# Optimization experiments

Measured on AMD Instinct MI355X. Metric: run time of the kernel, lower is better.

Reference implementation:

```python
import jax, jax.numpy as jnp
import numpy as np

N_NODES = 100000
N_EDGES = 1600000
D_FEAT = 64


def setup_inputs() -> dict:
    key = jax.random.key(0)
    k1, k2, k3, k4 = jax.random.split(key, 4)
    x = jax.random.normal(k1, (N_NODES, D_FEAT), dtype=jnp.float32)
    edge_values = jax.random.uniform(k2, (N_EDGES,), dtype=jnp.float32)
    # row-sorted targets mimic a coalesced sparse COO matrix
    target_index = jnp.sort(jax.random.randint(k3, (N_EDGES,), 0, N_NODES, dtype=jnp.int32))
    source_index = jax.random.randint(k4, (N_EDGES,), 0, N_NODES, dtype=jnp.int32)
    return {"x": x, "edge_values": edge_values,
            "target_index": target_index, "source_index": source_index}


def reference(x, edge_values, target_index, source_index):
    # sparsify_message: gather source rows -> [n_edges, d]
    msg = x[source_index]
    # scale by sparse neighborhood values
    msg = edge_values[:, None] * msg
    # aggregate: scatter-sum into target cells -> [n_nodes, d]
    out = jax.ops.segment_sum(msg, target_index, num_segments=N_NODES)
    return out
```

## Files before the change

kernel.cpp:

```cpp
#include <hip/hip_runtime.h>
#include <hip/hip_fp16.h>

#define N_NODES 100000
#define N_EDGES 1600000
#define D_FEAT 64

typedef __attribute__((ext_vector_type(4))) _Float16 half4v;

__global__ __launch_bounds__(256) void prep_kernel(
    const float4* __restrict__ x4,
    const int*    __restrict__ tgt,
    half4v*       __restrict__ xh,
    int*          __restrict__ row_ptr,
    int conv_blocks)
{
    const int bid = blockIdx.x;
    if (bid < conv_blocks) {
        int i = bid * 256 + threadIdx.x;
        if (i < N_NODES * 16) {
            float4 v = x4[i];
            half4v h;
            h.x = (_Float16)v.x; h.y = (_Float16)v.y;
            h.z = (_Float16)v.z; h.w = (_Float16)v.w;
            xh[i] = h;
        }
    } else {
        int e = (bid - conv_blocks) * 256 + threadIdx.x;
        if (e >= N_EDGES) return;
        int cur = tgt[e];
        int lo  = (e == 0) ? 0 : tgt[e - 1] + 1;
        for (int n = lo; n <= cur; ++n) row_ptr[n] = e;
        if (e == N_EDGES - 1) {
            for (int n = cur + 1; n <= N_NODES; ++n) row_ptr[n] = N_EDGES;
        }
    }
}

__global__ __launch_bounds__(256) void build_row_ptr(
    const int* __restrict__ tgt, int* __restrict__ row_ptr)
{
    int e = blockIdx.x * blockDim.x + threadIdx.x;
    if (e >= N_EDGES) return;
    int cur = tgt[e];
    int lo  = (e == 0) ? 0 : tgt[e - 1] + 1;
    for (int n = lo; n <= cur; ++n) row_ptr[n] = e;
    if (e == N_EDGES - 1) {
        for (int n = cur + 1; n <= N_NODES; ++n) row_ptr[n] = N_EDGES;
    }
}

__global__ __launch_bounds__(256) void gather_sum_h(
    const half4v* __restrict__ xh,
    const float*  __restrict__ ev,
    const int*    __restrict__ src,
    const int*    __restrict__ row_ptr,
    float4*       __restrict__ out4)
{
    const int node = blockIdx.x * 4 + (threadIdx.x >> 6);
    if (node >= N_NODES) return;
    const int lane = threadIdx.x & 63;
    const int g    = lane >> 4;
    const int f    = lane & 15;

    const int start = row_ptr[node];
    const int end   = row_ptr[node + 1];

    float4 acc = make_float4(0.f, 0.f, 0.f, 0.f);

    if (start < end) {
        int  ea = start + g, eb = start + 4 + g;
        bool va = ea < end,  vb = eb < end;
        int  esa = va ? ea : start, esb = vb ? eb : start;
        float wa = va ? ev[esa] : 0.0f;
        float wb = vb ? ev[esb] : 0.0f;
        int   sa = src[esa];
        int   sb = src[esb];

        for (int e0 = start; e0 < end; e0 += 8) {
            const half4v xa = xh[sa * 16 + f];
            const half4v xb = xh[sb * 16 + f];
            const float cwa = wa, cwb = wb;

            {
                int  na = e0 + 8 + g, nb = e0 + 12 + g;
                bool vna = na < end,  vnb = nb < end;
                int  nsa = vna ? na : start, nsb = vnb ? nb : start;
                wa = vna ? ev[nsa] : 0.0f;
                wb = vnb ? ev[nsb] : 0.0f;
                sa = src[nsa];
                sb = src[nsb];
            }

            acc.x = fmaf(cwa, (float)xa.x, acc.x);
            acc.y = fmaf(cwa, (float)xa.y, acc.y);
            acc.z = fmaf(cwa, (float)xa.z, acc.z);
            acc.w = fmaf(cwa, (float)xa.w, acc.w);
            acc.x = fmaf(cwb, (float)xb.x, acc.x);
            acc.y = fmaf(cwb, (float)xb.y, acc.y);
            acc.z = fmaf(cwb, (float)xb.z, acc.z);
            acc.w = fmaf(cwb, (float)xb.w, acc.w);
        }
    }

    acc.x += __shfl_xor(acc.x, 16, 64);
    acc.y += __shfl_xor(acc.y, 16, 64);
    acc.z += __shfl_xor(acc.z, 16, 64);
    acc.w += __shfl_xor(acc.w, 16, 64);
    acc.x += __shfl_xor(acc.x, 32, 64);
    acc.y += __shfl_xor(acc.y, 32, 64);
    acc.z += __shfl_xor(acc.z, 32, 64);
    acc.w += __shfl_xor(acc.w, 32, 64);

    if (g == 0) out4[node * 16 + f] = acc;
}

__global__ __launch_bounds__(256) void gather_sum_f32(
    const float4* __restrict__ x4,
    const float*  __restrict__ ev,
    const int*    __restrict__ src,
    const int*    __restrict__ row_ptr,
    float4*       __restrict__ out4)
{
    const int node = blockIdx.x * 4 + (threadIdx.x >> 6);
    if (node >= N_NODES) return;
    const int lane = threadIdx.x & 63;
    const int g    = lane >> 4;
    const int f    = lane & 15;

    const int start = row_ptr[node];
    const int end   = row_ptr[node + 1];

    float4 acc = make_float4(0.f, 0.f, 0.f, 0.f);
    if (start < end) {
        int  ea = start + g, eb = start + 4 + g;
        bool va = ea < end,  vb = eb < end;
        int  esa = va ? ea : start, esb = vb ? eb : start;
        float wa = va ? ev[esa] : 0.0f;
        float wb = vb ? ev[esb] : 0.0f;
        int   sa = src[esa];
        int   sb = src[esb];

        for (int e0 = start; e0 < end; e0 += 8) {
            const float4 xa = x4[sa * 16 + f];
            const float4 xb = x4[sb * 16 + f];
            const float cwa = wa, cwb = wb;
            {
                int  na = e0 + 8 + g, nb = e0 + 12 + g;
                bool vna = na < end,  vnb = nb < end;
                int  nsa = vna ? na : start, nsb = vnb ? nb : start;
                wa = vna ? ev[nsa] : 0.0f;
                wb = vnb ? ev[nsb] : 0.0f;
                sa = src[nsa];
                sb = src[nsb];
            }
            acc.x = fmaf(cwa, xa.x, acc.x);
            acc.y = fmaf(cwa, xa.y, acc.y);
            acc.z = fmaf(cwa, xa.z, acc.z);
            acc.w = fmaf(cwa, xa.w, acc.w);
            acc.x = fmaf(cwb, xb.x, acc.x);
            acc.y = fmaf(cwb, xb.y, acc.y);
            acc.z = fmaf(cwb, xb.z, acc.z);
            acc.w = fmaf(cwb, xb.w, acc.w);
        }
    }
    acc.x += __shfl_xor(acc.x, 16, 64);
    acc.y += __shfl_xor(acc.y, 16, 64);
    acc.z += __shfl_xor(acc.z, 16, 64);
    acc.w += __shfl_xor(acc.w, 16, 64);
    acc.x += __shfl_xor(acc.x, 32, 64);
    acc.y += __shfl_xor(acc.y, 32, 64);
    acc.z += __shfl_xor(acc.z, 32, 64);
    acc.w += __shfl_xor(acc.w, 32, 64);
    if (g == 0) out4[node * 16 + f] = acc;
}

extern "C" void kernel_launch(void* const* d_in, const int* in_sizes, int n_in,
                              void* d_out, int out_size, void* d_ws, size_t ws_size,
                              hipStream_t stream) {
    const float* x            = (const float*)d_in[0];
    const float* edge_values  = (const float*)d_in[1];
    const int*   target_index = (const int*)d_in[2];
    const int*   source_index = (const int*)d_in[3];
    float*       out          = (float*)d_out;

    const size_t rp_bytes = (size_t)(N_NODES + 1) * sizeof(int);
    const size_t xh_off   = (rp_bytes + 511) & ~(size_t)511;
    const size_t xh_bytes = (size_t)N_NODES * D_FEAT * sizeof(_Float16);
    const size_t need     = xh_off + xh_bytes;

    int* row_ptr = (int*)d_ws;

    if (ws_size >= need) {
        half4v* xh = (half4v*)((char*)d_ws + xh_off);
        const int conv_blocks = (N_NODES * 16 + 255) / 256;
        const int rp_blocks   = (N_EDGES + 255) / 256;
        prep_kernel<<<conv_blocks + rp_blocks, 256, 0, stream>>>(
            (const float4*)x, target_index, xh, row_ptr, conv_blocks);

        gather_sum_h<<<(N_NODES + 3) / 4, 256, 0, stream>>>(
            xh, edge_values, source_index, row_ptr, (float4*)out);
    } else {
        build_row_ptr<<<(N_EDGES + 255) / 256, 256, 0, stream>>>(target_index, row_ptr);
        gather_sum_f32<<<(N_NODES + 3) / 4, 256, 0, stream>>>(
            (const float4*)x, edge_values, source_index, row_ptr, (float4*)out);
    }
}
```

Measured before the change: 134.5 us.

## Map one 16-lane group per node and stage edge metadata through LDS

The half-precision gather kernel now assigns a 16-thread group to each node (16 nodes per block) in place of a full 64-lane wavefront. Each group loads up to 16 edges' source indices and weights cooperatively, stages them in shared memory, then issues four row gathers per step with software prefetching. This removes the cross-group shuffle reduction and the idle lanes on low-degree nodes, and quadruples nodes per block. In exchange each lane walks the edges serially, and the LDS exchange relies on implicit intra-wavefront ordering with no barrier.

```diff
diff --git a/kernel.cpp b/kernel.cpp
--- a/kernel.cpp
+++ b/kernel.cpp
@@ -49,6 +49,9 @@
     }
 }
 
+#define GROUPS_PER_BLOCK 16
+#define LDS_STRIDE_B     144
+
 __global__ __launch_bounds__(256) void gather_sum_h(
     const half4v* __restrict__ xh,
     const float*  __restrict__ ev,
@@ -56,62 +59,88 @@
     const int*    __restrict__ row_ptr,
     float4*       __restrict__ out4)
 {
-    const int node = blockIdx.x * 4 + (threadIdx.x >> 6);
+    __shared__ char lds_raw[GROUPS_PER_BLOCK * LDS_STRIDE_B];
+
+    const int tib  = threadIdx.x;
+    const int gib  = tib >> 4;
+    const int lane = tib & 15;
+    const int node = blockIdx.x * GROUPS_PER_BLOCK + gib;
     if (node >= N_NODES) return;
-    const int lane = threadIdx.x & 63;
-    const int g    = lane >> 4;
-    const int f    = lane & 15;
+
+    char* gbase = lds_raw + gib * LDS_STRIDE_B;
 
     const int start = row_ptr[node];
     const int end   = row_ptr[node + 1];
 
     float4 acc = make_float4(0.f, 0.f, 0.f, 0.f);
 
-    if (start < end) {
-        int  ea = start + g, eb = start + 4 + g;
-        bool va = ea < end,  vb = eb < end;
-        int  esa = va ? ea : start, esb = vb ? eb : start;
-        float wa = va ? ev[esa] : 0.0f;
-        float wb = vb ? ev[esb] : 0.0f;
-        int   sa = src[esa];
-        int   sb = src[esb];
-
-        for (int e0 = start; e0 < end; e0 += 8) {
-            const half4v xa = xh[sa * 16 + f];
-            const half4v xb = xh[sb * 16 + f];
-            const float cwa = wa, cwb = wb;
-
-            {
-                int  na = e0 + 8 + g, nb = e0 + 12 + g;
-                bool vna = na < end,  vnb = nb < end;
-                int  nsa = vna ? na : start, nsb = vnb ? nb : start;
-                wa = vna ? ev[nsa] : 0.0f;
-                wb = vnb ? ev[nsb] : 0.0f;
-                sa = src[nsa];
-                sb = src[nsb];
-            }
-
-            acc.x = fmaf(cwa, (float)xa.x, acc.x);
-            acc.y = fmaf(cwa, (float)xa.y, acc.y);
-            acc.z = fmaf(cwa, (float)xa.z, acc.z);
-            acc.w = fmaf(cwa, (float)xa.w, acc.w);
-            acc.x = fmaf(cwb, (float)xb.x, acc.x);
-            acc.y = fmaf(cwb, (float)xb.y, acc.y);
-            acc.z = fmaf(cwb, (float)xb.z, acc.z);
-            acc.w = fmaf(cwb, (float)xb.w, acc.w);
-        }
-    }
-
-    acc.x += __shfl_xor(acc.x, 16, 64);
-    acc.y += __shfl_xor(acc.y, 16, 64);
-    acc.z += __shfl_xor(acc.z, 16, 64);
-    acc.w += __shfl_xor(acc.w, 16, 64);
-    acc.x += __shfl_xor(acc.x, 32, 64);
-    acc.y += __shfl_xor(acc.y, 32, 64);
-    acc.z += __shfl_xor(acc.z, 32, 64);
-    acc.w += __shfl_xor(acc.w, 32, 64);
-
-    if (g == 0) out4[node * 16 + f] = acc;
+    for (int blk = start; blk < end; blk += 16) {
+        const int bcnt = end - blk;
+
+        int   s_ = 0; float w_ = 0.0f;
+        if (lane < bcnt) { s_ = src[blk + lane]; w_ = ev[blk + lane]; }
+        ((int2*)gbase)[lane] = make_int2(s_, __float_as_int(w_));
+
+        const int nch = (min(bcnt, 16) + 3) >> 2;
+
+        int4 m01 = ((const int4*)gbase)[0];
+        int4 m23 = ((const int4*)gbase)[1];
+        half4v x0 = xh[m01.x * 16 + lane];
+        half4v x1 = xh[m01.z * 16 + lane];
+        half4v x2 = xh[m23.x * 16 + lane];
+        half4v x3 = xh[m23.z * 16 + lane];
+        float w0 = __int_as_float(m01.y), w1 = __int_as_float(m01.w);
+        float w2 = __int_as_float(m23.y), w3 = __int_as_float(m23.w);
+
+        for (int c = 1; c < nch; ++c) {
+            int4 n01 = ((const int4*)gbase)[2 * c];
+            int4 n23 = ((const int4*)gbase)[2 * c + 1];
+            half4v nx0 = xh[n01.x * 16 + lane];
+            half4v nx1 = xh[n01.z * 16 + lane];
+            half4v nx2 = xh[n23.x * 16 + lane];
+            half4v nx3 = xh[n23.z * 16 + lane];
+
+            acc.x = fmaf(w0, (float)x0.x, acc.x);
+            acc.y = fmaf(w0, (float)x0.y, acc.y);
+            acc.z = fmaf(w0, (float)x0.z, acc.z);
+            acc.w = fmaf(w0, (float)x0.w, acc.w);
+            acc.x = fmaf(w1, (float)x1.x, acc.x);
+            acc.y = fmaf(w1, (float)x1.y, acc.y);
+            acc.z = fmaf(w1, (float)x1.z, acc.z);
+            acc.w = fmaf(w1, (float)x1.w, acc.w);
+            acc.x = fmaf(w2, (float)x2.x, acc.x);
+            acc.y = fmaf(w2, (float)x2.y, acc.y);
+            acc.z = fmaf(w2, (float)x2.z, acc.z);
+            acc.w = fmaf(w2, (float)x2.w, acc.w);
+            acc.x = fmaf(w3, (float)x3.x, acc.x);
+            acc.y = fmaf(w3, (float)x3.y, acc.y);
+            acc.z = fmaf(w3, (float)x3.z, acc.z);
+            acc.w = fmaf(w3, (float)x3.w, acc.w);
+
+            x0 = nx0; x1 = nx1; x2 = nx2; x3 = nx3;
+            w0 = __int_as_float(n01.y); w1 = __int_as_float(n01.w);
+            w2 = __int_as_float(n23.y); w3 = __int_as_float(n23.w);
+        }
+
+        acc.x = fmaf(w0, (float)x0.x, acc.x);
+        acc.y = fmaf(w0, (float)x0.y, acc.y);
+        acc.z = fmaf(w0, (float)x0.z, acc.z);
+        acc.w = fmaf(w0, (float)x0.w, acc.w);
+        acc.x = fmaf(w1, (float)x1.x, acc.x);
+        acc.y = fmaf(w1, (float)x1.y, acc.y);
+        acc.z = fmaf(w1, (float)x1.z, acc.z);
+        acc.w = fmaf(w1, (float)x1.w, acc.w);
+        acc.x = fmaf(w2, (float)x2.x, acc.x);
+        acc.y = fmaf(w2, (float)x2.y, acc.y);
+        acc.z = fmaf(w2, (float)x2.z, acc.z);
+        acc.w = fmaf(w2, (float)x2.w, acc.w);
+        acc.x = fmaf(w3, (float)x3.x, acc.x);
+        acc.y = fmaf(w3, (float)x3.y, acc.y);
+        acc.z = fmaf(w3, (float)x3.z, acc.z);
+        acc.w = fmaf(w3, (float)x3.w, acc.w);
+    }
+
+    out4[node * 16 + lane] = acc;
 }
 
 __global__ __launch_bounds__(256) void gather_sum_f32(
@@ -197,7 +226,8 @@
         prep_kernel<<<conv_blocks + rp_blocks, 256, 0, stream>>>(
             (const float4*)x, target_index, xh, row_ptr, conv_blocks);
 
-        gather_sum_h<<<(N_NODES + 3) / 4, 256, 0, stream>>>(
+        const int n_blocks = (N_NODES + GROUPS_PER_BLOCK - 1) / GROUPS_PER_BLOCK;
+        gather_sum_h<<<n_blocks, 256, 0, stream>>>(
             xh, edge_values, source_index, row_ptr, (float4*)out);
     } else {
         build_row_ptr<<<(N_EDGES + 255) / 256, 256, 0, stream>>>(target_index, row_ptr);
```

Result: faster. 120.8 us, median of 2 (-10.2%).

## Use 8-lane groups per node with LDS-staged edge indices and half8 gathers

Applied to the files above, without the earlier changes.

Changes the fp16 gather kernel from 64 lanes per node to 8 lanes per node, so each block handles 32 nodes and each lane loads 16-byte half8 vectors. Source indices and weights for up to 32 edges are loaded cooperatively and staged in LDS, then walked with a software-pipelined loop that prefetches the next four rows. The cross-lane shuffle reduction goes away, and far fewer lanes sit idle on nodes with few edges (about 16 per node). In exchange there is LDS traffic, per-lane serial loops over edges, and no explicit barrier around the LDS use (each 8-lane group uses only its own slice).

```diff
diff --git a/kernel.cpp b/kernel.cpp
--- a/kernel.cpp
+++ b/kernel.cpp
@@ -6,6 +6,7 @@
 #define D_FEAT 64
 
 typedef __attribute__((ext_vector_type(4))) _Float16 half4v;
+typedef __attribute__((ext_vector_type(8))) _Float16 half8v;
 
 __global__ __launch_bounds__(256) void prep_kernel(
     const float4* __restrict__ x4,
@@ -49,69 +50,101 @@
     }
 }
 
-__global__ __launch_bounds__(256) void gather_sum_h(
-    const half4v* __restrict__ xh,
+#define GPB        32
+#define LDS_STRIDE 272
+
+__global__ __launch_bounds__(256, 8) void gather_sum_h(
+    const half8v* __restrict__ xh8,
     const float*  __restrict__ ev,
     const int*    __restrict__ src,
     const int*    __restrict__ row_ptr,
     float4*       __restrict__ out4)
 {
-    const int node = blockIdx.x * 4 + (threadIdx.x >> 6);
+    __shared__ char lds_raw[GPB * LDS_STRIDE];
+
+    const int tib  = threadIdx.x;
+    const int gib  = tib >> 3;
+    const int lane = tib & 7;
+    const int node = blockIdx.x * GPB + gib;
     if (node >= N_NODES) return;
-    const int lane = threadIdx.x & 63;
-    const int g    = lane >> 4;
-    const int f    = lane & 15;
+
+    char* gbase = lds_raw + gib * LDS_STRIDE;
 
     const int start = row_ptr[node];
     const int end   = row_ptr[node + 1];
 
-    float4 acc = make_float4(0.f, 0.f, 0.f, 0.f);
-
-    if (start < end) {
-        int  ea = start + g, eb = start + 4 + g;
-        bool va = ea < end,  vb = eb < end;
-        int  esa = va ? ea : start, esb = vb ? eb : start;
-        float wa = va ? ev[esa] : 0.0f;
-        float wb = vb ? ev[esb] : 0.0f;
-        int   sa = src[esa];
-        int   sb = src[esb];
-
-        for (int e0 = start; e0 < end; e0 += 8) {
-            const half4v xa = xh[sa * 16 + f];
-            const half4v xb = xh[sb * 16 + f];
-            const float cwa = wa, cwb = wb;
-
-            {
-                int  na = e0 + 8 + g, nb = e0 + 12 + g;
-                bool vna = na < end,  vnb = nb < end;
-                int  nsa = vna ? na : start, nsb = vnb ? nb : start;
-                wa = vna ? ev[nsa] : 0.0f;
-                wb = vnb ? ev[nsb] : 0.0f;
-                sa = src[nsa];
-                sb = src[nsb];
-            }
-
-            acc.x = fmaf(cwa, (float)xa.x, acc.x);
-            acc.y = fmaf(cwa, (float)xa.y, acc.y);
-            acc.z = fmaf(cwa, (float)xa.z, acc.z);
-            acc.w = fmaf(cwa, (float)xa.w, acc.w);
-            acc.x = fmaf(cwb, (float)xb.x, acc.x);
-            acc.y = fmaf(cwb, (float)xb.y, acc.y);
-            acc.z = fmaf(cwb, (float)xb.z, acc.z);
-            acc.w = fmaf(cwb, (float)xb.w, acc.w);
-        }
-    }
-
-    acc.x += __shfl_xor(acc.x, 16, 64);
-    acc.y += __shfl_xor(acc.y, 16, 64);
-    acc.z += __shfl_xor(acc.z, 16, 64);
-    acc.w += __shfl_xor(acc.w, 16, 64);
-    acc.x += __shfl_xor(acc.x, 32, 64);
-    acc.y += __shfl_xor(acc.y, 32, 64);
-    acc.z += __shfl_xor(acc.z, 32, 64);
-    acc.w += __shfl_xor(acc.w, 32, 64);
-
-    if (g == 0) out4[node * 16 + f] = acc;
+    float4 accA = make_float4(0.f, 0.f, 0.f, 0.f);
+    float4 accB = make_float4(0.f, 0.f, 0.f, 0.f);
+
+#define ACC8(W, X) do { \
+        accA.x = fmaf((W), (float)(X)[0], accA.x); \
+        accA.y = fmaf((W), (float)(X)[1], accA.y); \
+        accA.z = fmaf((W), (float)(X)[2], accA.z); \
+        accA.w = fmaf((W), (float)(X)[3], accA.w); \
+        accB.x = fmaf((W), (float)(X)[4], accB.x); \
+        accB.y = fmaf((W), (float)(X)[5], accB.y); \
+        accB.z = fmaf((W), (float)(X)[6], accB.z); \
+        accB.w = fmaf((W), (float)(X)[7], accB.w); } while (0)
+
+    for (int blk = start; blk < end; blk += 32) {
+        {
+            const int e0   = blk + 4 * lane;
+            const int emax = end - 1;
+            int c0 = e0     < emax ? e0     : emax;
+            int c1 = e0 + 1 < emax ? e0 + 1 : emax;
+            int c2 = e0 + 2 < emax ? e0 + 2 : emax;
+            int c3 = e0 + 3 < emax ? e0 + 3 : emax;
+            int s0 = src[c0], s1 = src[c1], s2 = src[c2], s3 = src[c3];
+            float w0 = ev[c0], w1 = ev[c1], w2 = ev[c2], w3 = ev[c3];
+            w0 = (e0     < end) ? w0 : 0.0f;
+            w1 = (e0 + 1 < end) ? w1 : 0.0f;
+            w2 = (e0 + 2 < end) ? w2 : 0.0f;
+            w3 = (e0 + 3 < end) ? w3 : 0.0f;
+            ((int4*)gbase)[2 * lane]     =
+                make_int4(s0, __float_as_int(w0), s1, __float_as_int(w1));
+            ((int4*)gbase)[2 * lane + 1] =
+                make_int4(s2, __float_as_int(w2), s3, __float_as_int(w3));
+        }
+
+        const int rem = end - blk;
+        const int nch = ((rem < 32 ? rem : 32) + 3) >> 2;
+
+        int4 p0 = ((const int4*)gbase)[0];
+        int4 p1 = ((const int4*)gbase)[1];
+        half8v xa0 = xh8[p0.x * 8 + lane];
+        half8v xb0 = xh8[p0.z * 8 + lane];
+        half8v xc0 = xh8[p1.x * 8 + lane];
+        half8v xd0 = xh8[p1.z * 8 + lane];
+
+        for (int c = 1; c < nch; ++c) {
+            int4 q0 = ((const int4*)gbase)[2 * c];
+            int4 q1 = ((const int4*)gbase)[2 * c + 1];
+            half8v xa1 = xh8[q0.x * 8 + lane];
+            half8v xb1 = xh8[q0.z * 8 + lane];
+            half8v xc1 = xh8[q1.x * 8 + lane];
+            half8v xd1 = xh8[q1.z * 8 + lane];
+
+            int4 m0 = ((const int4*)gbase)[2 * (c - 1)];
+            int4 m1 = ((const int4*)gbase)[2 * (c - 1) + 1];
+            ACC8(__int_as_float(m0.y), xa0);
+            ACC8(__int_as_float(m0.w), xb0);
+            ACC8(__int_as_float(m1.y), xc0);
+            ACC8(__int_as_float(m1.w), xd0);
+
+            xa0 = xa1; xb0 = xb1; xc0 = xc1; xd0 = xd1;
+        }
+
+        int4 m0 = ((const int4*)gbase)[2 * (nch - 1)];
+        int4 m1 = ((const int4*)gbase)[2 * (nch - 1) + 1];
+        ACC8(__int_as_float(m0.y), xa0);
+        ACC8(__int_as_float(m0.w), xb0);
+        ACC8(__int_as_float(m1.y), xc0);
+        ACC8(__int_as_float(m1.w), xd0);
+    }
+#undef ACC8
+
+    out4[node * 16 + lane * 2]     = accA;
+    out4[node * 16 + lane * 2 + 1] = accB;
 }
 
 __global__ __launch_bounds__(256) void gather_sum_f32(
@@ -197,8 +230,9 @@
         prep_kernel<<<conv_blocks + rp_blocks, 256, 0, stream>>>(
             (const float4*)x, target_index, xh, row_ptr, conv_blocks);
 
-        gather_sum_h<<<(N_NODES + 3) / 4, 256, 0, stream>>>(
-            xh, edge_values, source_index, row_ptr, (float4*)out);
+        const int n_blocks = (N_NODES + GPB - 1) / GPB;
+        gather_sum_h<<<n_blocks, 256, 0, stream>>>(
+            (const half8v*)xh, edge_values, source_index, row_ptr, (float4*)out);
     } else {
         build_row_ptr<<<(N_EDGES + 255) / 256, 256, 0, stream>>>(target_index, row_ptr);
         gather_sum_f32<<<(N_NODES + 3) / 4, 256, 0, stream>>>(
```

Measured after the change: 121.3 us. -9.8%, faster.
